# Optimization experiments

Measured on AMD Instinct MI355X. Metric: run time of the kernel, lower is better.

Reference implementation:

```python
import jax, jax.numpy as jnp
import numpy as np

EPS = 1e-5

def _conv1x1(x, w, b):
    # x: [B,C,H,W], w: [O,C], b: [O]
    return jnp.einsum('bchw,oc->bohw', x, w) + b[None, :, None, None]

def setup_inputs() -> dict:
    key = jax.random.key(0)
    ks = jax.random.split(key, 6)
    B, C, H, W = 8, 512, 64, 64
    Ck, Cv, Co = 256, 256, 512
    x = jax.random.normal(ks[0], (B, C, H, W), dtype=jnp.float32)
    Wk = jax.random.normal(ks[1], (Ck, C), dtype=jnp.float32) * 0.02
    bk = jnp.zeros((Ck,), dtype=jnp.float32)
    gamma = jnp.ones((Ck,), dtype=jnp.float32)
    beta = jnp.zeros((Ck,), dtype=jnp.float32)
    Wv = jax.random.normal(ks[2], (Cv, C), dtype=jnp.float32) * 0.02
    bv = jnp.zeros((Cv,), dtype=jnp.float32)
    Ww = jax.random.normal(ks[3], (Co, Cv), dtype=jnp.float32) * 0.02
    bw = jnp.zeros((Co,), dtype=jnp.float32)
    return {'x': x, 'Wk': Wk, 'bk': bk, 'gamma': gamma, 'beta': beta,
            'Wv': Wv, 'bv': bv, 'Ww': Ww, 'bw': bw}

def reference(x, Wk, bk, gamma, beta, Wv, bv, Ww, bw):
    B, C, H, W = x.shape
    # f_key == f_query (shared module): conv1x1 -> BN (training stats) -> ReLU
    qk = _conv1x1(x, Wk, bk)                      # [B,Ck,H,W]
    mean = qk.mean(axis=(0, 2, 3))
    var = qk.var(axis=(0, 2, 3))                  # biased variance, as torch BN training
    feat = jax.nn.relu((qk - mean[None, :, None, None])
                       * jax.lax.rsqrt(var + EPS)[None, :, None, None]
                       * gamma[None, :, None, None] + beta[None, :, None, None])
    value = _conv1x1(x, Wv, bv)                   # [B,Cv,H,W]
    Ck = feat.shape[1]
    Cv = value.shape[1]
    N = H * W
    q = feat.reshape(B, Ck, N).transpose(0, 2, 1)  # [B,N,Ck]
    k = feat.reshape(B, Ck, N)                     # [B,Ck,N]
    v = value.reshape(B, Cv, N).transpose(0, 2, 1) # [B,N,Cv]
    scale = Ck ** (-0.5)
    sim = jax.nn.softmax(jnp.matmul(q, k) * scale, axis=-1)  # [B,N,N]
    ctx = jnp.matmul(sim, v)                       # [B,N,Cv]
    ctx = ctx.transpose(0, 2, 1).reshape(B, Cv, H, W)
    out = _conv1x1(ctx, Ww, bw)                    # [B,Co,H,W]
    # scale==1 -> visualize_* upsamples are identity; sim_map visual is None
    return (out, feat, feat, value)
```

## Files before the change

### kernel.cpp

```cpp
#include <hip/hip_runtime.h>
#include <math.h>

constexpr int  Bn  = 8;
constexpr int  Cin = 512;
constexpr int  Nn  = 4096;
constexpr int  Ck  = 256;
constexpr int  Cv  = 256;
constexpr int  Co  = 512;

constexpr size_t F1_OFF  = (size_t)Bn * Co * Nn;
constexpr size_t F2_OFF  = F1_OFF + (size_t)Bn * Ck * Nn;
constexpr size_t VAL_OFF = F2_OFF + (size_t)Bn * Ck * Nn;

typedef __attribute__((ext_vector_type(8)))  short  short8;
typedef __attribute__((ext_vector_type(16))) float  f32x16;
typedef __attribute__((ext_vector_type(8)))  ushort ushort8;

static __device__ __forceinline__ ushort f2bf(float f) {
    union { float f; unsigned u; } x; x.f = f;
    unsigned r = x.u + 0x7fffu + ((x.u >> 16) & 1u);
    return (ushort)(r >> 16);
}

static __device__ __forceinline__ void gll16(const void* g, void* l) {
    __builtin_amdgcn_global_load_lds(
        (const __attribute__((address_space(1))) void*)g,
        (__attribute__((address_space(3))) void*)l, 16, 0, 0);
}

__global__ __launch_bounds__(256) void cast_w(const float* __restrict__ a,
                                              const float* __restrict__ b,
                                              const float* __restrict__ c,
                                              ushort* __restrict__ da,
                                              ushort* __restrict__ db,
                                              ushort* __restrict__ dc)
{
    const int tid   = blockIdx.x * 256 + threadIdx.x;
    const int which = tid >> 14;
    const int off   = (tid & 16383) * 8;
    const float* s = (which == 0) ? a : (which == 1) ? b : c;
    ushort*      d = (which == 0) ? da : (which == 1) ? db : dc;
    const float4 u = *(const float4*)(s + off);
    const float4 v = *(const float4*)(s + off + 4);
    ushort8 o;
    o[0] = f2bf(u.x); o[1] = f2bf(u.y); o[2] = f2bf(u.z); o[3] = f2bf(u.w);
    o[4] = f2bf(v.x); o[5] = f2bf(v.y); o[6] = f2bf(v.z); o[7] = f2bf(v.w);
    *(ushort8*)(d + off) = o;
}

__global__ __launch_bounds__(256) void transpose_c(const float* __restrict__ src,
                                                   ushort* __restrict__ dst, int C)
{
    const int b  = blockIdx.z;
    const int c0 = blockIdx.y * 64;
    const int n0 = blockIdx.x * 64;
    const int t  = threadIdx.x;
    __shared__ float T[64][65];
#pragma unroll
    for (int p = 0; p < 4; ++p) {
        const int flat = p * 256 + t;
        const int cc = flat >> 4, nn4 = (flat & 15) * 4;
        const float4 v = *(const float4*)(
            src + ((size_t)b * C + c0 + cc) * Nn + n0 + nn4);
        T[cc][nn4]     = v.x; T[cc][nn4 + 1] = v.y;
        T[cc][nn4 + 2] = v.z; T[cc][nn4 + 3] = v.w;
    }
    __syncthreads();
#pragma unroll
    for (int p = 0; p < 2; ++p) {
        const int flat = p * 256 + t;
        const int nn = flat >> 3, cc0 = (flat & 7) * 8;
        ushort8 o;
#pragma unroll
        for (int i = 0; i < 8; ++i) o[i] = f2bf(T[cc0 + i][nn]);
        *(ushort8*)(dst + ((size_t)b * Nn + n0 + nn) * C + c0 + cc0) = o;
    }
}

template <int K, bool DUAL>
__global__ __launch_bounds__(256) void gemm_bf(const ushort* __restrict__ XT,
                                               const ushort* __restrict__ Wb,
                                               const float*  __restrict__ bias,
                                               float* __restrict__ out,
                                               ushort* __restrict__ out_bf,
                                               int M)
{
    const int b  = blockIdx.z;
    const int m0 = blockIdx.y * 128;
    const int n0 = blockIdx.x * 128;
    const int t  = threadIdx.x;
    const int w  = t >> 6, L = t & 63;
    const int l31 = L & 31, hl = L >> 5;
    const int wm = (w >> 1) * 64, wn = (w & 1) * 64;

    __shared__ __align__(16) short As[128][72];
    __shared__ __align__(16) short Bs[128][72];

    const ushort* Xb = XT + (size_t)b * Nn * K;

    f32x16 acc[2][2];
#pragma unroll
    for (int a = 0; a < 2; ++a)
#pragma unroll
        for (int bb = 0; bb < 2; ++bb)
#pragma unroll
            for (int r = 0; r < 16; ++r) acc[a][bb][r] = 0.f;

    for (int k0 = 0; k0 < K; k0 += 64) {
        __syncthreads();
#pragma unroll
        for (int p = 0; p < 4; ++p) {
            const int e   = p * 256 + t;
            const int row = e >> 3, ko = (e & 7) * 8;
            *(short8*)&As[row][ko] =
                *(const short8*)(Wb + (size_t)(m0 + row) * K + k0 + ko);
            *(short8*)&Bs[row][ko] =
                *(const short8*)(Xb + (size_t)(n0 + row) * K + k0 + ko);
        }
        __syncthreads();
#pragma unroll
        for (int kc = 0; kc < 4; ++kc) {
            short8 Af[2], Bf[2];
#pragma unroll
            for (int a = 0; a < 2; ++a)
                Af[a] = *(const short8*)&As[wm + a * 32 + l31][kc * 16 + hl * 8];
#pragma unroll
            for (int bb = 0; bb < 2; ++bb)
                Bf[bb] = *(const short8*)&Bs[wn + bb * 32 + l31][kc * 16 + hl * 8];
#pragma unroll
            for (int a = 0; a < 2; ++a)
#pragma unroll
                for (int bb = 0; bb < 2; ++bb)
                    acc[a][bb] = __builtin_amdgcn_mfma_f32_32x32x16_bf16(
                        Af[a], Bf[bb], acc[a][bb], 0, 0, 0);
        }
    }

#pragma unroll
    for (int a = 0; a < 2; ++a)
#pragma unroll
        for (int r = 0; r < 16; ++r) {
            const int row = (r & 3) + 8 * (r >> 2) + 4 * hl;
            const int o   = m0 + wm + a * 32 + row;
            const float bv = bias[o];
            const size_t base = ((size_t)b * M + o) * Nn + n0 + wn + l31;
#pragma unroll
            for (int bb = 0; bb < 2; ++bb) {
                const float vv = acc[a][bb][r] + bv;
                out[base + bb * 32] = vv;
                if (DUAL) out_bf[base + bb * 32] = f2bf(vv);
            }
        }
}

__global__ __launch_bounds__(256) void bn_stats(const float* __restrict__ qk,
                                                const float* __restrict__ gamma,
                                                const float* __restrict__ beta,
                                                float* __restrict__ ss)
{
    const int o = blockIdx.x;
    const int t = threadIdx.x;
    float s = 0.f, sq = 0.f;
    for (int b = 0; b < Bn; ++b) {
        const float* p = qk + ((size_t)b * Ck + o) * Nn;
        for (int n = t * 4; n < Nn; n += 1024) {
            const float4 v = *(const float4*)(p + n);
            s  += v.x + v.y + v.z + v.w;
            sq += v.x * v.x + v.y * v.y + v.z * v.z + v.w * v.w;
        }
    }
    __shared__ float rs[256], rq[256];
    rs[t] = s; rq[t] = sq;
    __syncthreads();
    for (int off = 128; off > 0; off >>= 1) {
        if (t < off) { rs[t] += rs[t + off]; rq[t] += rq[t + off]; }
        __syncthreads();
    }
    if (t == 0) {
        const float cnt  = (float)(Bn * Nn);
        const float mean = rs[0] / cnt;
        const float var  = rq[0] / cnt - mean * mean;
        const float inv  = rsqrtf(var + 1e-5f);
        const float sc   = gamma[o] * inv;
        ss[o]       = sc;
        ss[256 + o] = beta[o] - mean * sc;
    }
}

__global__ __launch_bounds__(256) void bn_relu(const float* __restrict__ qk,
                                               const float* __restrict__ ss,
                                               float* __restrict__ f1,
                                               float* __restrict__ f2)
{
    const size_t tid = (size_t)blockIdx.x * 256 + threadIdx.x;
    const size_t idx = tid * 4;
    const int o = (int)((idx >> 12) & 255);
    const float sc = ss[o], sh = ss[256 + o];
    const float4 v = *(const float4*)(qk + idx);
    float4 r;
    r.x = fmaxf(v.x * sc + sh, 0.f);
    r.y = fmaxf(v.y * sc + sh, 0.f);
    r.z = fmaxf(v.z * sc + sh, 0.f);
    r.w = fmaxf(v.w * sc + sh, 0.f);
    *(float4*)(f1 + idx) = r;
    *(float4*)(f2 + idx) = r;
}

constexpr int LDS_BYTES = 163840;

__global__ __launch_bounds__(512) void attn_mfma(const ushort* __restrict__ featT,
                                                 const ushort* __restrict__ valB,
                                                 ushort* __restrict__ ctx)
{
    extern __shared__ __align__(16) char lds[];
    char* ldsK = lds;
    char* ldsV = lds + 65536;
    char* ldsP = lds + 131072;

    const int b   = blockIdx.x;
    const int i0  = blockIdx.y * 128;
    const int t   = threadIdx.x;
    const int w   = t >> 6;
    const int L   = t & 63;
    const int l31 = L & 31, hl = L >> 5;
    const int ig  = w >> 1;
    const int ch  = w & 1;
    const int jsel = ch * 32;

    const int rbK  = hl * 16 + (((jsel + l31) << 4) & 511);
    const int rotV = (l31 << 4) & 127;

    const ushort* F = featT + (size_t)b * Nn * Ck;
    const ushort* V = valB  + (size_t)b * Cv * Nn;
    const char*   Vg = (const char*)V;

    constexpr float CEXP = 0.09016844005556021f;
    constexpr int NT = Nn / 64;

#define STAGE_K(J0, BUF) do {                                                  \
        const char* Kg_ = (const char*)(F + (size_t)(J0) * Ck);                \
        char* Kd_ = ldsK + (BUF) * 32768;                                      \
        _Pragma("unroll")                                                      \
        for (int p_ = 0; p_ < 4; ++p_) {                                       \
            const int c_ = w * 4 + p_;                                         \
            const int o_ = c_ * 1024 + L * 16;                                 \
            const int rK_ = o_ >> 9;                                           \
            gll16(Kg_ + rK_ * 512 + ((o_ - rK_ * 16) & 511), Kd_ + c_ * 1024); \
        }                                                                      \
    } while (0)

#define STAGE_V(J0, BUF) do {                                                  \
        char* Vd_ = ldsV + (BUF) * 32768;                                      \
        _Pragma("unroll")                                                      \
        for (int p_ = 0; p_ < 4; ++p_) {                                       \
            const int c_ = w * 4 + p_;                                         \
            const int o_ = c_ * 1024 + L * 16;                                 \
            const int rV_ = o_ >> 7;                                           \
            gll16(Vg + (size_t)rV_ * (Nn * 2) + (size_t)(J0) * 2               \
                     + ((o_ - rV_ * 16) & 127), Vd_ + c_ * 1024);              \
        }                                                                      \
    } while (0)

    STAGE_K(0, 0);
    short8 Qf[16];
    {
        const ushort* qp = F + ((size_t)(i0 + ig * 32 + l31)) * Ck + hl * 8;
#pragma unroll
        for (int kc = 0; kc < 16; ++kc)
            Qf[kc] = *(const short8*)(qp + kc * 16);
    }
    asm volatile("s_waitcnt vmcnt(0)" ::: "memory");
    __builtin_amdgcn_s_barrier();

    f32x16 Oacc[4];
#pragma unroll
    for (int c = 0; c < 4; ++c)
#pragma unroll
        for (int r = 0; r < 16; ++r) Oacc[c][r] = 0.f;
    float lsum = 0.f;
    short8 PfA{}, PfB{};

    int cur = 0;
    for (int s = 0; s < NT; ++s) {
        const int jn = (s + 1 < NT ? s + 1 : NT - 1) * 64;
        STAGE_K(jn, cur ^ 1);
        STAGE_V((size_t)s * 64, cur);

        const char* Kr = ldsK + cur * 32768 + (jsel + l31) * 512;
        f32x16 Sa, Sb;
#pragma unroll
        for (int r = 0; r < 16; ++r) { Sa[r] = 0.f; Sb[r] = 0.f; }
        __builtin_amdgcn_s_setprio(1);
#pragma unroll
        for (int kc = 0; kc < 8; ++kc) {
            const short8 K0 = *(const short8*)(Kr + ((kc * 64      + rbK) & 511));
            const short8 K1 = *(const short8*)(Kr + ((kc * 64 + 32 + rbK) & 511));
            Sa = __builtin_amdgcn_mfma_f32_32x32x16_bf16(K0, Qf[2 * kc],     Sa, 0, 0, 0);
            Sb = __builtin_amdgcn_mfma_f32_32x32x16_bf16(K1, Qf[2 * kc + 1], Sb, 0, 0, 0);
        }
        __builtin_amdgcn_s_setprio(0);

        if (s > 0) {
            const char* Vr2 = ldsV + (cur ^ 1) * 32768 + (ch * 128 + l31) * 128;
            const char* Pr  = ldsP + (cur ^ 1) * 16384
                              + ((ig * 4 + (ch ^ 1) * 2) * 2 + hl) * 512 + l31 * 16;
            const short8 Po0 = *(const short8*)(Pr);
            const short8 Po1 = *(const short8*)(Pr + 1024);
            __builtin_amdgcn_s_setprio(1);
#pragma unroll
            for (int g = 0; g < 2; ++g) {
                const short8 Pa = g ? PfB : PfA;
                const int jbyte = (ch * 2 + g) * 32 + hl * 16;
#pragma unroll
                for (int cvt = 0; cvt < 4; ++cvt) {
                    const short8 Vf = *(const short8*)(Vr2 + cvt * 4096
                                         + ((jbyte + rotV) & 127));
                    Oacc[cvt] = __builtin_amdgcn_mfma_f32_32x32x16_bf16(
                        Pa, Vf, Oacc[cvt], 0, 0, 0);
                }
            }
#pragma unroll
            for (int g = 0; g < 2; ++g) {
                const short8 Pa = g ? Po1 : Po0;
                const int jbyte = ((ch ^ 1) * 2 + g) * 32 + hl * 16;
#pragma unroll
                for (int cvt = 0; cvt < 4; ++cvt) {
                    const short8 Vf = *(const short8*)(Vr2 + cvt * 4096
                                         + ((jbyte + rotV) & 127));
                    Oacc[cvt] = __builtin_amdgcn_mfma_f32_32x32x16_bf16(
                        Pa, Vf, Oacc[cvt], 0, 0, 0);
                }
            }
            __builtin_amdgcn_s_setprio(0);
        }

        unsigned pw[8];
#pragma unroll
        for (int r2 = 0; r2 < 8; ++r2) {
            const float p0 = exp2f((Sa[2 * r2]     + Sb[2 * r2])     * CEXP);
            const float p1 = exp2f((Sa[2 * r2 + 1] + Sb[2 * r2 + 1]) * CEXP);
            const unsigned u0 = (unsigned)f2bf(p0);
            const unsigned u1 = (unsigned)f2bf(p1);
            lsum += __uint_as_float(u0 << 16) + __uint_as_float(u1 << 16);
            pw[r2] = u0 | (u1 << 16);
        }
        {
            char* Pw = ldsP + cur * 16384
                       + ((ig * 4 + ch * 2) * 2 + hl) * 512 + l31 * 16;
            short8 nf[2];
#pragma unroll
            for (int g = 0; g < 2; ++g) {
                auto s02 = __builtin_amdgcn_permlane32_swap(pw[4 * g + 0], pw[4 * g + 2],
                                                            false, false);
                auto s13 = __builtin_amdgcn_permlane32_swap(pw[4 * g + 1], pw[4 * g + 3],
                                                            false, false);
                union { unsigned u[4]; short8 s; } pu;
                pu.u[0] = s02[0]; pu.u[1] = s13[0]; pu.u[2] = s02[1]; pu.u[3] = s13[1];
                nf[g] = pu.s;
                *(short8*)(Pw + g * 1024) = pu.s;
            }
            PfA = nf[0]; PfB = nf[1];
        }

        asm volatile("s_waitcnt vmcnt(0) lgkmcnt(0)" ::: "memory");
        __builtin_amdgcn_s_barrier();
        cur ^= 1;
    }
#undef STAGE_K
#undef STAGE_V

    {
        const char* Vr2 = ldsV + (cur ^ 1) * 32768 + (ch * 128 + l31) * 128;
        const char* Pr  = ldsP + (cur ^ 1) * 16384
                          + ((ig * 4 + (ch ^ 1) * 2) * 2 + hl) * 512 + l31 * 16;
        const short8 Po0 = *(const short8*)(Pr);
        const short8 Po1 = *(const short8*)(Pr + 1024);
#pragma unroll
        for (int g = 0; g < 2; ++g) {
            const short8 Pa = g ? PfB : PfA;
            const int jbyte = (ch * 2 + g) * 32 + hl * 16;
#pragma unroll
            for (int cvt = 0; cvt < 4; ++cvt) {
                const short8 Vf = *(const short8*)(Vr2 + cvt * 4096
                                     + ((jbyte + rotV) & 127));
                Oacc[cvt] = __builtin_amdgcn_mfma_f32_32x32x16_bf16(
                    Pa, Vf, Oacc[cvt], 0, 0, 0);
            }
        }
#pragma unroll
        for (int g = 0; g < 2; ++g) {
            const short8 Pa = g ? Po1 : Po0;
            const int jbyte = ((ch ^ 1) * 2 + g) * 32 + hl * 16;
#pragma unroll
            for (int cvt = 0; cvt < 4; ++cvt) {
                const short8 Vf = *(const short8*)(Vr2 + cvt * 4096
                                     + ((jbyte + rotV) & 127));
                Oacc[cvt] = __builtin_amdgcn_mfma_f32_32x32x16_bf16(
                    Pa, Vf, Oacc[cvt], 0, 0, 0);
            }
        }
    }

    {
        unsigned a = __float_as_uint(lsum), bcopy = a;
        auto sw = __builtin_amdgcn_permlane32_swap(a, bcopy, false, false);
        lsum = __uint_as_float(sw[0]) + __uint_as_float(sw[1]);
    }
    float* Lr = (float*)ldsP;
    Lr[(ig * 2 + ch) * 32 + l31] = lsum;
    asm volatile("s_waitcnt lgkmcnt(0)" ::: "memory");
    __builtin_amdgcn_s_barrier();

    ushort* Cb = ctx + ((size_t)b * Nn + i0 + ig * 32) * Cv + ch * 128;
#pragma unroll
    for (int r = 0; r < 16; ++r) {
        const int row = (r & 3) + 8 * (r >> 2) + 4 * hl;
        const float lt = Lr[(ig * 2) * 32 + row] + Lr[(ig * 2 + 1) * 32 + row];
        const float linv = 1.f / lt;
        ushort* cp = Cb + (size_t)row * Cv + l31;
#pragma unroll
        for (int c4 = 0; c4 < 4; ++c4)
            cp[c4 * 32] = f2bf(Oacc[c4][r] * linv);
    }
}

extern "C" void kernel_launch(void* const* d_in, const int* in_sizes, int n_in,
                              void* d_out, int out_size, void* d_ws, size_t ws_size,
                              hipStream_t stream)
{
    const float* x     = (const float*)d_in[0];
    const float* Wk    = (const float*)d_in[1];
    const float* bk    = (const float*)d_in[2];
    const float* gamma = (const float*)d_in[3];
    const float* beta  = (const float*)d_in[4];
    const float* Wv    = (const float*)d_in[5];
    const float* bv    = (const float*)d_in[6];
    const float* Ww    = (const float*)d_in[7];
    const float* bw    = (const float*)d_in[8];

    float* out = (float*)d_out;
    float* f1  = out + F1_OFF;
    float* f2  = out + F2_OFF;
    float* val = out + VAL_OFF;

    ushort* xT    = (ushort*)d_ws;
    ushort* featT = xT;
    ushort* ctxb  = xT + (size_t)8388608;
    ushort* valB  = xT + (size_t)16777216;
    ushort* Wkb   = valB + (size_t)8388608;
    ushort* Wvb   = Wkb + 131072;
    ushort* Wwb   = Wvb + 131072;
    float*  ss    = (float*)(Wwb + 131072);

    static bool attn_attr_set = false;
    if (!attn_attr_set) {
        (void)hipFuncSetAttribute((const void*)attn_mfma,
                                  hipFuncAttributeMaxDynamicSharedMemorySize,
                                  LDS_BYTES);
        attn_attr_set = true;
    }

    cast_w<<<192, 256, 0, stream>>>(Wk, Wv, Ww, Wkb, Wvb, Wwb);
    transpose_c<<<dim3(Nn / 64, Cin / 64, Bn), 256, 0, stream>>>(x, xT, Cin);
    gemm_bf<512, false><<<dim3(Nn / 128, Ck / 128, Bn), 256, 0, stream>>>(
        xT, Wkb, bk, f1, nullptr, Ck);
    gemm_bf<512, true><<<dim3(Nn / 128, Cv / 128, Bn), 256, 0, stream>>>(
        xT, Wvb, bv, val, valB, Cv);
    bn_stats<<<Ck, 256, 0, stream>>>(f1, gamma, beta, ss);
    bn_relu<<<(Bn * Ck * Nn) / (256 * 4), 256, 0, stream>>>(f1, ss, f1, f2);
    transpose_c<<<dim3(Nn / 64, Ck / 64, Bn), 256, 0, stream>>>(f1, featT, Ck);
    attn_mfma<<<dim3(Bn, Nn / 128), 512, LDS_BYTES, stream>>>(featT, valB, ctxb);
    gemm_bf<256, false><<<dim3(Nn / 128, Co / 128, Bn), 256, 0, stream>>>(
        ctxb, Wwb, bw, out, nullptr, Co);
}
```

Baseline: 475.1 us.

## Fuse key/value GEMMs, fuse BN-ReLU with transpose, simplify attention P reuse

Merges the key and value 1x1-conv GEMMs into one kernel that shares the staged input tile, so x is read from memory once for both projections. Fuses the BN-ReLU apply with the bf16 transpose that builds featT, which removes one full read of the feature tensor and one launch. In the attention kernel, P fragments are now re-read from LDS rather than kept in registers, the row sum uses unrounded probabilities, and the bf16 packing uses v_cvt_pk_bf16_f32. The fused GEMM doubles accumulator registers, which may lower occupancy.

Result: faster. 438.1 us (-7.8%).

```diff
diff --git a/kernel.cpp b/kernel.cpp
--- a/kernel.cpp
+++ b/kernel.cpp
@@ -77,13 +77,14 @@
     }
 }
 
-template <int K, bool DUAL>
-__global__ __launch_bounds__(256) void gemm_bf(const ushort* __restrict__ XT,
-                                               const ushort* __restrict__ Wb,
-                                               const float*  __restrict__ bias,
-                                               float* __restrict__ out,
-                                               ushort* __restrict__ out_bf,
-                                               int M)
+__global__ __launch_bounds__(256) void gemm_qv(const ushort* __restrict__ XT,
+                                               const ushort* __restrict__ Wkb,
+                                               const ushort* __restrict__ Wvb,
+                                               const float*  __restrict__ bk,
+                                               const float*  __restrict__ bv,
+                                               float* __restrict__ qk,
+                                               float* __restrict__ val,
+                                               ushort* __restrict__ valB)
 {
     const int b  = blockIdx.z;
     const int m0 = blockIdx.y * 128;
@@ -93,46 +94,54 @@
     const int l31 = L & 31, hl = L >> 5;
     const int wm = (w >> 1) * 64, wn = (w & 1) * 64;
 
-    __shared__ __align__(16) short As[128][72];
+    __shared__ __align__(16) short AsK[128][72];
+    __shared__ __align__(16) short AsV[128][72];
     __shared__ __align__(16) short Bs[128][72];
 
-    const ushort* Xb = XT + (size_t)b * Nn * K;
-
-    f32x16 acc[2][2];
+    const ushort* Xb = XT + (size_t)b * Nn * Cin;
+
+    f32x16 accK[2][2], accV[2][2];
 #pragma unroll
     for (int a = 0; a < 2; ++a)
 #pragma unroll
         for (int bb = 0; bb < 2; ++bb)
 #pragma unroll
-            for (int r = 0; r < 16; ++r) acc[a][bb][r] = 0.f;
-
-    for (int k0 = 0; k0 < K; k0 += 64) {
+            for (int r = 0; r < 16; ++r) { accK[a][bb][r] = 0.f; accV[a][bb][r] = 0.f; }
+
+    for (int k0 = 0; k0 < Cin; k0 += 64) {
         __syncthreads();
 #pragma unroll
         for (int p = 0; p < 4; ++p) {
             const int e   = p * 256 + t;
             const int row = e >> 3, ko = (e & 7) * 8;
-            *(short8*)&As[row][ko] =
-                *(const short8*)(Wb + (size_t)(m0 + row) * K + k0 + ko);
+            *(short8*)&AsK[row][ko] =
+                *(const short8*)(Wkb + (size_t)(m0 + row) * Cin + k0 + ko);
+            *(short8*)&AsV[row][ko] =
+                *(const short8*)(Wvb + (size_t)(m0 + row) * Cin + k0 + ko);
             *(short8*)&Bs[row][ko] =
-                *(const short8*)(Xb + (size_t)(n0 + row) * K + k0 + ko);
+                *(const short8*)(Xb + (size_t)(n0 + row) * Cin + k0 + ko);
         }
         __syncthreads();
 #pragma unroll
         for (int kc = 0; kc < 4; ++kc) {
-            short8 Af[2], Bf[2];
-#pragma unroll
-            for (int a = 0; a < 2; ++a)
-                Af[a] = *(const short8*)&As[wm + a * 32 + l31][kc * 16 + hl * 8];
+            short8 Ak[2], Av[2], Bf[2];
+#pragma unroll
+            for (int a = 0; a < 2; ++a) {
+                Ak[a] = *(const short8*)&AsK[wm + a * 32 + l31][kc * 16 + hl * 8];
+                Av[a] = *(const short8*)&AsV[wm + a * 32 + l31][kc * 16 + hl * 8];
+            }
 #pragma unroll
             for (int bb = 0; bb < 2; ++bb)
                 Bf[bb] = *(const short8*)&Bs[wn + bb * 32 + l31][kc * 16 + hl * 8];
 #pragma unroll
             for (int a = 0; a < 2; ++a)
 #pragma unroll
-                for (int bb = 0; bb < 2; ++bb)
-                    acc[a][bb] = __builtin_amdgcn_mfma_f32_32x32x16_bf16(
-                        Af[a], Bf[bb], acc[a][bb], 0, 0, 0);
+                for (int bb = 0; bb < 2; ++bb) {
+                    accK[a][bb] = __builtin_amdgcn_mfma_f32_32x32x16_bf16(
+                        Ak[a], Bf[bb], accK[a][bb], 0, 0, 0);
+                    accV[a][bb] = __builtin_amdgcn_mfma_f32_32x32x16_bf16(
+                        Av[a], Bf[bb], accV[a][bb], 0, 0, 0);
+                }
         }
     }
 
@@ -142,13 +151,14 @@
         for (int r = 0; r < 16; ++r) {
             const int row = (r & 3) + 8 * (r >> 2) + 4 * hl;
             const int o   = m0 + wm + a * 32 + row;
-            const float bv = bias[o];
-            const size_t base = ((size_t)b * M + o) * Nn + n0 + wn + l31;
+            const float bkv = bk[o], bvv = bv[o];
+            const size_t base = ((size_t)b * Ck + o) * Nn + n0 + wn + l31;
 #pragma unroll
             for (int bb = 0; bb < 2; ++bb) {
-                const float vv = acc[a][bb][r] + bv;
-                out[base + bb * 32] = vv;
-                if (DUAL) out_bf[base + bb * 32] = f2bf(vv);
+                qk[base + bb * 32] = accK[a][bb][r] + bkv;
+                const float vv = accV[a][bb][r] + bvv;
+                val[base + bb * 32]  = vv;
+                valB[base + bb * 32] = f2bf(vv);
             }
         }
 }
@@ -187,23 +197,44 @@
     }
 }
 
-__global__ __launch_bounds__(256) void bn_relu(const float* __restrict__ qk,
-                                               const float* __restrict__ ss,
-                                               float* __restrict__ f1,
-                                               float* __restrict__ f2)
-{
-    const size_t tid = (size_t)blockIdx.x * 256 + threadIdx.x;
-    const size_t idx = tid * 4;
-    const int o = (int)((idx >> 12) & 255);
-    const float sc = ss[o], sh = ss[256 + o];
-    const float4 v = *(const float4*)(qk + idx);
-    float4 r;
-    r.x = fmaxf(v.x * sc + sh, 0.f);
-    r.y = fmaxf(v.y * sc + sh, 0.f);
-    r.z = fmaxf(v.z * sc + sh, 0.f);
-    r.w = fmaxf(v.w * sc + sh, 0.f);
-    *(float4*)(f1 + idx) = r;
-    *(float4*)(f2 + idx) = r;
+__global__ __launch_bounds__(256) void bn_relu_t(const float* __restrict__ qk,
+                                                 const float* __restrict__ ss,
+                                                 float* __restrict__ f1,
+                                                 float* __restrict__ f2,
+                                                 ushort* __restrict__ featT)
+{
+    const int b  = blockIdx.z;
+    const int c0 = blockIdx.y * 64;
+    const int n0 = blockIdx.x * 64;
+    const int t  = threadIdx.x;
+    __shared__ float T[64][65];
+#pragma unroll
+    for (int p = 0; p < 4; ++p) {
+        const int flat = p * 256 + t;
+        const int cc = flat >> 4, nn4 = (flat & 15) * 4;
+        const size_t gidx = ((size_t)b * Ck + c0 + cc) * Nn + n0 + nn4;
+        const float sc = ss[c0 + cc], sh = ss[256 + c0 + cc];
+        const float4 v = *(const float4*)(qk + gidx);
+        float4 r;
+        r.x = fmaxf(v.x * sc + sh, 0.f);
+        r.y = fmaxf(v.y * sc + sh, 0.f);
+        r.z = fmaxf(v.z * sc + sh, 0.f);
+        r.w = fmaxf(v.w * sc + sh, 0.f);
+        *(float4*)(f1 + gidx) = r;
+        *(float4*)(f2 + gidx) = r;
+        T[cc][nn4]     = r.x; T[cc][nn4 + 1] = r.y;
+        T[cc][nn4 + 2] = r.z; T[cc][nn4 + 3] = r.w;
+    }
+    __syncthreads();
+#pragma unroll
+    for (int p = 0; p < 2; ++p) {
+        const int flat = p * 256 + t;
+        const int nn = flat >> 3, cc0 = (flat & 7) * 8;
+        ushort8 o;
+#pragma unroll
+        for (int i = 0; i < 8; ++i) o[i] = f2bf(T[cc0 + i][nn]);
+        *(ushort8*)(featT + ((size_t)b * Nn + n0 + nn) * Ck + c0 + cc0) = o;
+    }
 }
 
 constexpr int LDS_BYTES = 163840;
@@ -278,7 +309,6 @@
 #pragma unroll
         for (int r = 0; r < 16; ++r) Oacc[c][r] = 0.f;
     float lsum = 0.f;
-    short8 PfA{}, PfB{};
 
     int cur = 0;
     for (int s = 0; s < NT; ++s) {
@@ -302,27 +332,12 @@
 
         if (s > 0) {
             const char* Vr2 = ldsV + (cur ^ 1) * 32768 + (ch * 128 + l31) * 128;
-            const char* Pr  = ldsP + (cur ^ 1) * 16384
-                              + ((ig * 4 + (ch ^ 1) * 2) * 2 + hl) * 512 + l31 * 16;
-            const short8 Po0 = *(const short8*)(Pr);
-            const short8 Po1 = *(const short8*)(Pr + 1024);
+            const char* Pr  = ldsP + (cur ^ 1) * 16384 + (ig * 8 + hl) * 512 + l31 * 16;
             __builtin_amdgcn_s_setprio(1);
 #pragma unroll
-            for (int g = 0; g < 2; ++g) {
-                const short8 Pa = g ? PfB : PfA;
-                const int jbyte = (ch * 2 + g) * 32 + hl * 16;
-#pragma unroll
-                for (int cvt = 0; cvt < 4; ++cvt) {
-                    const short8 Vf = *(const short8*)(Vr2 + cvt * 4096
-                                         + ((jbyte + rotV) & 127));
-                    Oacc[cvt] = __builtin_amdgcn_mfma_f32_32x32x16_bf16(
-                        Pa, Vf, Oacc[cvt], 0, 0, 0);
-                }
-            }
-#pragma unroll
-            for (int g = 0; g < 2; ++g) {
-                const short8 Pa = g ? Po1 : Po0;
-                const int jbyte = ((ch ^ 1) * 2 + g) * 32 + hl * 16;
+            for (int jb = 0; jb < 4; ++jb) {
+                const short8 Pa = *(const short8*)(Pr + jb * 1024);
+                const int jbyte = jb * 32 + hl * 16;
 #pragma unroll
                 for (int cvt = 0; cvt < 4; ++cvt) {
                     const short8 Vf = *(const short8*)(Vr2 + cvt * 4096
@@ -339,15 +354,14 @@
         for (int r2 = 0; r2 < 8; ++r2) {
             const float p0 = exp2f((Sa[2 * r2]     + Sb[2 * r2])     * CEXP);
             const float p1 = exp2f((Sa[2 * r2 + 1] + Sb[2 * r2 + 1]) * CEXP);
-            const unsigned u0 = (unsigned)f2bf(p0);
-            const unsigned u1 = (unsigned)f2bf(p1);
-            lsum += __uint_as_float(u0 << 16) + __uint_as_float(u1 << 16);
-            pw[r2] = u0 | (u1 << 16);
+            lsum += p0 + p1;
+            unsigned pk;
+            asm("v_cvt_pk_bf16_f32 %0, %1, %2" : "=v"(pk) : "v"(p0), "v"(p1));
+            pw[r2] = pk;
         }
         {
             char* Pw = ldsP + cur * 16384
                        + ((ig * 4 + ch * 2) * 2 + hl) * 512 + l31 * 16;
-            short8 nf[2];
 #pragma unroll
             for (int g = 0; g < 2; ++g) {
                 auto s02 = __builtin_amdgcn_permlane32_swap(pw[4 * g + 0], pw[4 * g + 2],
@@ -356,10 +370,8 @@
                                                             false, false);
                 union { unsigned u[4]; short8 s; } pu;
                 pu.u[0] = s02[0]; pu.u[1] = s13[0]; pu.u[2] = s02[1]; pu.u[3] = s13[1];
-                nf[g] = pu.s;
                 *(short8*)(Pw + g * 1024) = pu.s;
             }
-            PfA = nf[0]; PfB = nf[1];
         }
 
         asm volatile("s_waitcnt vmcnt(0) lgkmcnt(0)" ::: "memory");
@@ -371,14 +383,11 @@
 
     {
         const char* Vr2 = ldsV + (cur ^ 1) * 32768 + (ch * 128 + l31) * 128;
-        const char* Pr  = ldsP + (cur ^ 1) * 16384
-                          + ((ig * 4 + (ch ^ 1) * 2) * 2 + hl) * 512 + l31 * 16;
-        const short8 Po0 = *(const short8*)(Pr);
-        const short8 Po1 = *(const short8*)(Pr + 1024);
-#pragma unroll
-        for (int g = 0; g < 2; ++g) {
-            const short8 Pa = g ? PfB : PfA;
-            const int jbyte = (ch * 2 + g) * 32 + hl * 16;
+        const char* Pr  = ldsP + (cur ^ 1) * 16384 + (ig * 8 + hl) * 512 + l31 * 16;
+#pragma unroll
+        for (int jb = 0; jb < 4; ++jb) {
+            const short8 Pa = *(const short8*)(Pr + jb * 1024);
+            const int jbyte = jb * 32 + hl * 16;
 #pragma unroll
             for (int cvt = 0; cvt < 4; ++cvt) {
                 const short8 Vf = *(const short8*)(Vr2 + cvt * 4096
@@ -387,18 +396,6 @@
                     Pa, Vf, Oacc[cvt], 0, 0, 0);
             }
         }
-#pragma unroll
-        for (int g = 0; g < 2; ++g) {
-            const short8 Pa = g ? Po1 : Po0;
-            const int jbyte = ((ch ^ 1) * 2 + g) * 32 + hl * 16;
-#pragma unroll
-            for (int cvt = 0; cvt < 4; ++cvt) {
-                const short8 Vf = *(const short8*)(Vr2 + cvt * 4096
-                                     + ((jbyte + rotV) & 127));
-                Oacc[cvt] = __builtin_amdgcn_mfma_f32_32x32x16_bf16(
-                    Pa, Vf, Oacc[cvt], 0, 0, 0);
-            }
-        }
     }
 
     {
@@ -422,6 +419,78 @@
         for (int c4 = 0; c4 < 4; ++c4)
             cp[c4 * 32] = f2bf(Oacc[c4][r] * linv);
     }
+}
+
+template <int K>
+__global__ __launch_bounds__(256) void gemm_bf(const ushort* __restrict__ XT,
+                                               const ushort* __restrict__ Wb,
+                                               const float*  __restrict__ bias,
+                                               float* __restrict__ out,
+                                               int M)
+{
+    const int b  = blockIdx.z;
+    const int m0 = blockIdx.y * 128;
+    const int n0 = blockIdx.x * 128;
+    const int t  = threadIdx.x;
+    const int w  = t >> 6, L = t & 63;
+    const int l31 = L & 31, hl = L >> 5;
+    const int wm = (w >> 1) * 64, wn = (w & 1) * 64;
+
+    __shared__ __align__(16) short As[128][72];
+    __shared__ __align__(16) short Bs[128][72];
+
+    const ushort* Xb = XT + (size_t)b * Nn * K;
+
+    f32x16 acc[2][2];
+#pragma unroll
+    for (int a = 0; a < 2; ++a)
+#pragma unroll
+        for (int bb = 0; bb < 2; ++bb)
+#pragma unroll
+            for (int r = 0; r < 16; ++r) acc[a][bb][r] = 0.f;
+
+    for (int k0 = 0; k0 < K; k0 += 64) {
+        __syncthreads();
+#pragma unroll
+        for (int p = 0; p < 4; ++p) {
+            const int e   = p * 256 + t;
+            const int row = e >> 3, ko = (e & 7) * 8;
+            *(short8*)&As[row][ko] =
+                *(const short8*)(Wb + (size_t)(m0 + row) * K + k0 + ko);
+            *(short8*)&Bs[row][ko] =
+                *(const short8*)(Xb + (size_t)(n0 + row) * K + k0 + ko);
+        }
+        __syncthreads();
+#pragma unroll
+        for (int kc = 0; kc < 4; ++kc) {
+            short8 Af[2], Bf[2];
+#pragma unroll
+            for (int a = 0; a < 2; ++a)
+                Af[a] = *(const short8*)&As[wm + a * 32 + l31][kc * 16 + hl * 8];
+#pragma unroll
+            for (int bb = 0; bb < 2; ++bb)
+                Bf[bb] = *(const short8*)&Bs[wn + bb * 32 + l31][kc * 16 + hl * 8];
+#pragma unroll
+            for (int a = 0; a < 2; ++a)
+#pragma unroll
+                for (int bb = 0; bb < 2; ++bb)
+                    acc[a][bb] = __builtin_amdgcn_mfma_f32_32x32x16_bf16(
+                        Af[a], Bf[bb], acc[a][bb], 0, 0, 0);
+        }
+    }
+
+#pragma unroll
+    for (int a = 0; a < 2; ++a)
+#pragma unroll
+        for (int r = 0; r < 16; ++r) {
+            const int row = (r & 3) + 8 * (r >> 2) + 4 * hl;
+            const int o   = m0 + wm + a * 32 + row;
+            const float bv = bias[o];
+            const size_t base = ((size_t)b * M + o) * Nn + n0 + wn + l31;
+#pragma unroll
+            for (int bb = 0; bb < 2; ++bb)
+                out[base + bb * 32] = acc[a][bb][r] + bv;
+        }
 }
 
 extern "C" void kernel_launch(void* const* d_in, const int* in_sizes, int n_in,
@@ -462,14 +531,12 @@
 
     cast_w<<<192, 256, 0, stream>>>(Wk, Wv, Ww, Wkb, Wvb, Wwb);
     transpose_c<<<dim3(Nn / 64, Cin / 64, Bn), 256, 0, stream>>>(x, xT, Cin);
-    gemm_bf<512, false><<<dim3(Nn / 128, Ck / 128, Bn), 256, 0, stream>>>(
-        xT, Wkb, bk, f1, nullptr, Ck);
-    gemm_bf<512, true><<<dim3(Nn / 128, Cv / 128, Bn), 256, 0, stream>>>(
-        xT, Wvb, bv, val, valB, Cv);
+    gemm_qv<<<dim3(Nn / 128, Ck / 128, Bn), 256, 0, stream>>>(
+        xT, Wkb, Wvb, bk, bv, f1, val, valB);
     bn_stats<<<Ck, 256, 0, stream>>>(f1, gamma, beta, ss);
-    bn_relu<<<(Bn * Ck * Nn) / (256 * 4), 256, 0, stream>>>(f1, ss, f1, f2);
-    transpose_c<<<dim3(Nn / 64, Ck / 64, Bn), 256, 0, stream>>>(f1, featT, Ck);
+    bn_relu_t<<<dim3(Nn / 64, Ck / 64, Bn), 256, 0, stream>>>(
+        f1, ss, f1, f2, featT);
     attn_mfma<<<dim3(Bn, Nn / 128), 512, LDS_BYTES, stream>>>(featT, valB, ctxb);
-    gemm_bf<256, false><<<dim3(Nn / 128, Co / 128, Bn), 256, 0, stream>>>(
-        ctxb, Wwb, bw, out, nullptr, Co);
-}
+    gemm_bf<256><<<dim3(Nn / 128, Co / 128, Bn), 256, 0, stream>>>(
+        ctxb, Wwb, bw, out, Co);
+}
```
